# Kernel tuning notes

Hardware: AMD Instinct MI355X
Metric: run time of the kernel (lower is better)

The kernel has to match this reference:

```python
import jax, jax.numpy as jnp
import numpy as np

N = 10000
IN_DIM = 256
HID = 64


def gcn_norm(edge_index, num_nodes):
    # PyG gcn_norm with add_remaining_self_loops: drop existing self-loops
    # (weight 0), append one self-loop per node with weight 1, then
    # symmetric deg^-1/2 normalization.
    src, dst = edge_index[0], edge_index[1]
    w = jnp.where(src == dst, 0.0, 1.0).astype(jnp.float32)
    loops = jnp.arange(num_nodes, dtype=src.dtype)
    src_f = jnp.concatenate([src, loops])
    dst_f = jnp.concatenate([dst, loops])
    w_f = jnp.concatenate([w, jnp.ones((num_nodes,), jnp.float32)])
    deg = jax.ops.segment_sum(w_f, dst_f, num_segments=num_nodes)
    dinv = jnp.where(deg > 0, jax.lax.rsqrt(deg), 0.0)
    norm = dinv[src_f] * w_f * dinv[dst_f]
    return src_f, dst_f, norm


def gcn_conv(x, W, b, src, dst, norm, num_nodes):
    xw = x @ W                      # [N, out]
    msg = xw[src] * norm[:, None]   # gather + scale
    out = jax.ops.segment_sum(msg, dst, num_segments=num_nodes)
    return out + b


def setup_inputs() -> dict:
    key = jax.random.key(0)
    ks = jax.random.split(key, 16)
    x = jax.random.normal(ks[0], (N, IN_DIM), jnp.float32)
    edge_index = jax.random.randint(ks[1], (2, 320000), 0, N, dtype=jnp.int64)
    s = 0.1
    return {
        "x": x,
        "edge_index": edge_index,
        # shared_encoder: 2 layers, in->hid, hid->hid
        "enc_W1": jax.random.normal(ks[2], (IN_DIM, HID), jnp.float32) * s,
        "enc_b1": jnp.zeros((HID,), jnp.float32),
        "enc_W2": jax.random.normal(ks[3], (HID, HID), jnp.float32) * s,
        "enc_b2": jnp.zeros((HID,), jnp.float32),
        # attr_decoder: 2 layers, hid->hid, hid->in
        "attr_W1": jax.random.normal(ks[4], (HID, HID), jnp.float32) * s,
        "attr_b1": jnp.zeros((HID,), jnp.float32),
        "attr_W2": jax.random.normal(ks[5], (HID, IN_DIM), jnp.float32) * s,
        "attr_b2": jnp.zeros((IN_DIM,), jnp.float32),
        # struct_decoder: 1 layer, hid->in
        "struct_W": jax.random.normal(ks[6], (HID, IN_DIM), jnp.float32) * s,
        "struct_b": jnp.zeros((IN_DIM,), jnp.float32),
    }


def reference(x, edge_index, enc_W1, enc_b1, enc_W2, enc_b2,
              attr_W1, attr_b1, attr_W2, attr_b2, struct_W, struct_b):
    src, dst, norm = gcn_norm(edge_index, N)

    # shared encoder (relu between layers, none after last; dropout=0 eval)
    h = gcn_conv(x, enc_W1, enc_b1, src, dst, norm, N)
    h = jax.nn.relu(h)
    h = gcn_conv(h, enc_W2, enc_b2, src, dst, norm, N)

    # attribute decoder
    x_ = gcn_conv(h, attr_W1, attr_b1, src, dst, norm, N)
    x_ = jax.nn.relu(x_)
    x_ = gcn_conv(x_, attr_W2, attr_b2, src, dst, norm, N)

    # structure decoder + dense adjacency reconstruction
    h_ = gcn_conv(h, struct_W, struct_b, src, dst, norm, N)
    adj_ = h_ @ h_.T  # [N, N]
    return (x_, adj_)
```

## Files before the change

### kernel.cpp

```cpp
#include <hip/hip_runtime.h>
#include <hip/hip_bf16.h>

#define NN 10000
#define INDIM 256
#define HIDDIM 64

typedef __hip_bfloat16 bf16;
typedef unsigned short u16;
typedef __attribute__((ext_vector_type(8))) short bf16x8;
typedef __attribute__((ext_vector_type(4))) float f32x4;

__global__ void k_sniff(const unsigned* __restrict__ xw, const unsigned* __restrict__ ew,
                        int* __restrict__ flags) {
    if (threadIdx.x == 0 && blockIdx.x == 0) {
        int c = 0;
        for (int j = 0; j < 256; ++j) {
            unsigned e = (xw[j] >> 7) & 0xFF;
            c += (e >= 0x74 && e <= 0x85);
        }
        flags[0] = (c >= 128);
        int z = 0;
        for (int j = 0; j < 128; ++j) z += (ew[2 * j + 1] == 0u);
        flags[1] = (z >= 64);
    }
}

__global__ void k_cvt(const void* __restrict__ in, float* __restrict__ out, int n,
                      const int* __restrict__ flags) {
    int i = blockIdx.x * 256 + threadIdx.x;
    if (i >= n) return;
    if (flags[0]) out[i] = __bfloat162float(((const bf16*)in)[i]);
    else          out[i] = ((const float*)in)[i];
}

__global__ void k_cvt_idx(const void* __restrict__ ei, int* __restrict__ s32,
                          int* __restrict__ d32, int E, const int* __restrict__ flags) {
    int e = blockIdx.x * 256 + threadIdx.x;
    if (e >= E) return;
    if (flags[1]) {
        const long long* p = (const long long*)ei;
        s32[e] = (int)p[e]; d32[e] = (int)p[e + E];
    } else {
        const int* p = (const int*)ei;
        s32[e] = p[e]; d32[e] = p[e + E];
    }
}


__global__ void k_init_deg(float* deg) {
    int i = blockIdx.x * 256 + threadIdx.x;
    if (i < NN) deg[i] = 1.0f;
}

__global__ void k_edge_deg(const int* __restrict__ src, const int* __restrict__ dst,
                           float* __restrict__ deg, int E) {
    int e = blockIdx.x * 256 + threadIdx.x;
    if (e < E) {
        int s = src[e], d = dst[e];
        if (s != d) atomicAdd(&deg[d], 1.0f);
    }
}

__global__ void k_dinv(float* deg, float* selfn) {
    int i = blockIdx.x * 256 + threadIdx.x;
    if (i < NN) {
        float dv = 1.0f / sqrtf(deg[i]);
        deg[i] = dv;
        selfn[i] = dv * dv;
    }
}

__global__ void k_edge_norm(const int* __restrict__ src, const int* __restrict__ dst,
                            const float* __restrict__ dinv, float* __restrict__ nrm, int E) {
    int e = blockIdx.x * 256 + threadIdx.x;
    if (e < E) {
        int s = src[e], d = dst[e];
        nrm[e] = (s != d) ? dinv[s] * dinv[d] : 0.0f;
    }
}


template <int K, int NOUT>
__global__ void k_gemm(const float* __restrict__ A, const float* __restrict__ W,
                       float* __restrict__ out) {
    int j = blockIdx.x * 64 + threadIdx.x;
    int i = blockIdx.y * 4 + threadIdx.y;
    const float* arow = A + (size_t)i * K;
    float acc = 0.0f;
#pragma unroll 8
    for (int k = 0; k < K; ++k)
        acc = fmaf(arow[k], W[k * NOUT + j], acc);
    out[(size_t)i * NOUT + j] = acc;
}

template <int K, int NOUT, bool RELU>
__global__ void k_gemm_bias(const float* __restrict__ A, const float* __restrict__ W,
                            const float* __restrict__ b, float* __restrict__ out) {
    int j = blockIdx.x * 64 + threadIdx.x;
    int i = blockIdx.y * 4 + threadIdx.y;
    const float* arow = A + (size_t)i * K;
    float acc = b[j];
#pragma unroll 8
    for (int k = 0; k < K; ++k)
        acc = fmaf(arow[k], W[k * NOUT + j], acc);
    if (RELU) acc = fmaxf(acc, 0.0f);
    out[(size_t)i * NOUT + j] = acc;
}

__global__ void k_gemm_split(const float* __restrict__ A, const float* __restrict__ W,
                             const float* __restrict__ b,
                             u16* __restrict__ hi, u16* __restrict__ lo) {
    int j = blockIdx.x * 64 + threadIdx.x;
    int i = blockIdx.y * 4 + threadIdx.y;
    size_t o = (size_t)i * 256 + j;
    const float* arow = A + (size_t)i * 64;
    float acc = b[j];
#pragma unroll 8
    for (int k = 0; k < 64; ++k)
        acc = fmaf(arow[k], W[k * 256 + j], acc);
    bf16 h = __float2bfloat16(acc);
    float hf = __bfloat162float(h);
    bf16 l = __float2bfloat16(acc - hf);
    hi[o] = *(const u16*)&h;
    lo[o] = *(const u16*)&l;
}

__global__ void k_gemm_out(const float* __restrict__ A, const float* __restrict__ W,
                           const float* __restrict__ b, void* __restrict__ out,
                           const int* __restrict__ flags) {
    int j = blockIdx.x * 64 + threadIdx.x;
    int i = blockIdx.y * 4 + threadIdx.y;
    const float* arow = A + (size_t)i * 64;
    float acc = b[j];
#pragma unroll 8
    for (int k = 0; k < 64; ++k)
        acc = fmaf(arow[k], W[k * 256 + j], acc);
    size_t o = (size_t)i * 256 + j;
    if (flags[0]) ((bf16*)out)[o] = __float2bfloat16(acc);
    else          ((float*)out)[o] = acc;
}


template <int F>
__global__ void k_agg_init(const float* __restrict__ xw, const float* __restrict__ selfn,
                           float* __restrict__ agg) {
    int t = blockIdx.x * 256 + threadIdx.x;
    int i = t / F;
    agg[t] = selfn[i] * xw[t];
}

template <int F>
__global__ void k_scatter(const int* __restrict__ src, const int* __restrict__ dst,
                          const float* __restrict__ nrm, const float* __restrict__ xw,
                          float* __restrict__ agg, int E) {
    int e = blockIdx.x * 4 + (threadIdx.x >> 6);
    int lane = threadIdx.x & 63;
    if (e < E) {
        float w = nrm[e];
        if (w != 0.0f) {
            const float* xs = xw + (size_t)src[e] * F;
            float* ad = agg + (size_t)dst[e] * F;
#pragma unroll
            for (int r = 0; r < F / 64; ++r) {
                int f = r * 64 + lane;
                atomicAdd(ad + f, w * xs[f]);
            }
        }
    }
}

template <int F, bool RELU>
__global__ void k_finalize_f32(const float* __restrict__ agg, const float* __restrict__ b,
                               float* __restrict__ out) {
    int t = blockIdx.x * 256 + threadIdx.x;
    float v = agg[t] + b[t & (F - 1)];
    if (RELU) v = fmaxf(v, 0.0f);
    out[t] = v;
}


__global__ __launch_bounds__(256) void k_adj_mfma(const u16* __restrict__ hi,
                                                  const u16* __restrict__ lo,
                                                  void* __restrict__ d_out,
                                                  const int* __restrict__ flags) {
    int wid  = threadIdx.x >> 6;
    int lane = threadIdx.x & 63;
    int wr = wid >> 1, wc = wid & 1;
    int row0 = blockIdx.y * 128 + wr * 64;
    int col0 = blockIdx.x * 128 + wc * 64;
    int lr  = lane & 15;
    int klo = (lane >> 4) * 8;

    int aoff[4], boff[4];
#pragma unroll
    for (int u = 0; u < 4; ++u) {
        int r = row0 + u * 16 + lr; if (r > NN - 1) r = NN - 1;
        aoff[u] = r * 256 + klo;
        int c = col0 + u * 16 + lr; if (c > NN - 1) c = NN - 1;
        boff[u] = c * 256 + klo;
    }

    f32x4 acc[4][4] = {};
    for (int k0 = 0; k0 < 256; k0 += 32) {
        bf16x8 ah[4], al[4], bh[4], bl[4];
#pragma unroll
        for (int u = 0; u < 4; ++u) {
            ah[u] = *(const bf16x8*)(hi + aoff[u] + k0);
            al[u] = *(const bf16x8*)(lo + aoff[u] + k0);
            bh[u] = *(const bf16x8*)(hi + boff[u] + k0);
            bl[u] = *(const bf16x8*)(lo + boff[u] + k0);
        }
#pragma unroll
        for (int u = 0; u < 4; ++u)
#pragma unroll
            for (int v = 0; v < 4; ++v) {
                acc[u][v] = __builtin_amdgcn_mfma_f32_16x16x32_bf16(ah[u], bh[v], acc[u][v], 0, 0, 0);
                acc[u][v] = __builtin_amdgcn_mfma_f32_16x16x32_bf16(ah[u], bl[v], acc[u][v], 0, 0, 0);
                acc[u][v] = __builtin_amdgcn_mfma_f32_16x16x32_bf16(al[u], bh[v], acc[u][v], 0, 0, 0);
            }
    }

    int obf = flags[0];
    int cr = (lane >> 4) * 4;
    int cc = lane & 15;
    bf16*  ob = (bf16*)d_out + (size_t)NN * INDIM;
    float* of = (float*)d_out + (size_t)NN * INDIM;
#pragma unroll
    for (int u = 0; u < 4; ++u) {
#pragma unroll
        for (int r = 0; r < 4; ++r) {
            int i = row0 + u * 16 + cr + r;
            if (i >= NN) continue;
#pragma unroll
            for (int v = 0; v < 4; ++v) {
                int j = col0 + v * 16 + cc;
                if (j >= NN) continue;
                float val = acc[u][v][r];
                if (obf) ob[(size_t)i * NN + j] = __float2bfloat16(val);
                else     of[(size_t)i * NN + j] = val;
            }
        }
    }
}


extern "C" void kernel_launch(void* const* d_in, const int* in_sizes, int n_in,
                              void* d_out, int out_size, void* d_ws, size_t ws_size,
                              hipStream_t stream) {
    const void* x_raw  = d_in[0];
    const void* ei_raw = d_in[1];

    const int E = in_sizes[1] / 2;

    int*   flags = (int*)d_ws;
    float* wsf   = (float*)d_ws;
    float* deg   = wsf + 16;
    float* selfn = wsf + 10256;
    float* nrm   = wsf + 20496;
    int*   s32   = (int*)(wsf + 348176);
    int*   d32   = (int*)(wsf + 668176);
    float* w32   = wsf + 988176;
    u16*   hs_hi = (u16*)(wsf + 1046560);
    u16*   hs_lo = hs_hi + (size_t)NN * 256;

    float* encW1 = w32 + 0;
    float* encb1 = w32 + 16384;
    float* encW2 = w32 + 16448;
    float* encb2 = w32 + 20544;
    float* attW1 = w32 + 20608;
    float* attb1 = w32 + 24704;
    float* attW2 = w32 + 24768;
    float* attb2 = w32 + 41152;
    float* stW   = w32 + 41408;
    float* stb   = w32 + 57792;

    float* osc  = (float*)((char*)d_out + 16000000);
    float* x32  = osc;
    float* bufA = osc + 2560000;
    float* bufB = osc + 5120000;
    float* h1   = osc + 7680000;
    float* h2   = osc + 8320000;
    float* a1   = osc + 8960000;

    int eb  = (E + 255) / 256;
    int ewb = (E + 3) / 4;

    k_sniff<<<1, 64, 0, stream>>>((const unsigned*)x_raw, (const unsigned*)ei_raw, flags);

    k_cvt<<<10000, 256, 0, stream>>>(x_raw, x32, NN * INDIM, flags);
    k_cvt<<<64, 256, 0, stream>>>(d_in[2],  encW1, 16384, flags);
    k_cvt<<<1, 256, 0, stream>>>(d_in[3],   encb1, 64, flags);
    k_cvt<<<16, 256, 0, stream>>>(d_in[4],  encW2, 4096, flags);
    k_cvt<<<1, 256, 0, stream>>>(d_in[5],   encb2, 64, flags);
    k_cvt<<<16, 256, 0, stream>>>(d_in[6],  attW1, 4096, flags);
    k_cvt<<<1, 256, 0, stream>>>(d_in[7],   attb1, 64, flags);
    k_cvt<<<64, 256, 0, stream>>>(d_in[8],  attW2, 16384, flags);
    k_cvt<<<1, 256, 0, stream>>>(d_in[9],   attb2, 256, flags);
    k_cvt<<<64, 256, 0, stream>>>(d_in[10], stW, 16384, flags);
    k_cvt<<<1, 256, 0, stream>>>(d_in[11],  stb, 256, flags);
    k_cvt_idx<<<eb, 256, 0, stream>>>(ei_raw, s32, d32, E, flags);

    k_init_deg<<<40, 256, 0, stream>>>(deg);
    k_edge_deg<<<eb, 256, 0, stream>>>(s32, d32, deg, E);
    k_dinv<<<40, 256, 0, stream>>>(deg, selfn);
    k_edge_norm<<<eb, 256, 0, stream>>>(s32, d32, deg, nrm, E);

    k_gemm<256, 64><<<dim3(1, 2500), dim3(64, 4), 0, stream>>>(x32, encW1, bufA);
    k_agg_init<64><<<2500, 256, 0, stream>>>(bufA, selfn, bufB);
    k_scatter<64><<<ewb, 256, 0, stream>>>(s32, d32, nrm, bufA, bufB, E);
    k_finalize_f32<64, true><<<2500, 256, 0, stream>>>(bufB, encb1, h1);

    k_agg_init<64><<<2500, 256, 0, stream>>>(h1, selfn, bufB);
    k_scatter<64><<<ewb, 256, 0, stream>>>(s32, d32, nrm, h1, bufB, E);
    k_gemm_bias<64, 64, false><<<dim3(1, 2500), dim3(64, 4), 0, stream>>>(bufB, encW2, encb2, h2);

    k_agg_init<64><<<2500, 256, 0, stream>>>(h2, selfn, bufB);
    k_scatter<64><<<ewb, 256, 0, stream>>>(s32, d32, nrm, h2, bufB, E);
    k_gemm_bias<64, 64, true><<<dim3(1, 2500), dim3(64, 4), 0, stream>>>(bufB, attW1, attb1, a1);
    k_gemm_split<<<dim3(4, 2500), dim3(64, 4), 0, stream>>>(bufB, stW, stb, hs_hi, hs_lo);

    k_agg_init<64><<<2500, 256, 0, stream>>>(a1, selfn, bufB);
    k_scatter<64><<<ewb, 256, 0, stream>>>(s32, d32, nrm, a1, bufB, E);
    k_gemm_out<<<dim3(4, 2500), dim3(64, 4), 0, stream>>>(bufB, attW2, attb2, d_out, flags);

    k_adj_mfma<<<dim3(79, 79), 256, 0, stream>>>(hs_hi, hs_lo, d_out, flags);
}
```

Measured before the change: 1.322 ms.

## Replace atomic edge scatter with CSR gather and vectorize adjacency stores

```diff
diff --git a/kernel.cpp b/kernel.cpp
--- a/kernel.cpp
+++ b/kernel.cpp
@@ -9,6 +9,7 @@
 typedef unsigned short u16;
 typedef __attribute__((ext_vector_type(8))) short bf16x8;
 typedef __attribute__((ext_vector_type(4))) float f32x4;
+typedef __attribute__((ext_vector_type(4))) unsigned short u16x4;
 
 __global__ void k_sniff(const unsigned* __restrict__ xw, const unsigned* __restrict__ ew,
                         int* __restrict__ flags) {
@@ -33,49 +34,71 @@
     else          out[i] = ((const float*)in)[i];
 }
 
-__global__ void k_cvt_idx(const void* __restrict__ ei, int* __restrict__ s32,
-                          int* __restrict__ d32, int E, const int* __restrict__ flags) {
+__global__ void k_zero(int* __restrict__ p, int n) {
+    int i = blockIdx.x * 256 + threadIdx.x;
+    if (i < n) p[i] = 0;
+}
+
+__global__ void k_cvt_idx_count(const void* __restrict__ ei, int* __restrict__ s32,
+                                int* __restrict__ d32, int* __restrict__ cnt,
+                                int E, const int* __restrict__ flags) {
     int e = blockIdx.x * 256 + threadIdx.x;
     if (e >= E) return;
+    int s, d;
     if (flags[1]) {
         const long long* p = (const long long*)ei;
-        s32[e] = (int)p[e]; d32[e] = (int)p[e + E];
+        s = (int)p[e]; d = (int)p[e + E];
     } else {
         const int* p = (const int*)ei;
-        s32[e] = p[e]; d32[e] = p[e + E];
-    }
-}
-
-
-__global__ void k_init_deg(float* deg) {
-    int i = blockIdx.x * 256 + threadIdx.x;
-    if (i < NN) deg[i] = 1.0f;
-}
-
-__global__ void k_edge_deg(const int* __restrict__ src, const int* __restrict__ dst,
-                           float* __restrict__ deg, int E) {
+        s = p[e]; d = p[e + E];
+    }
+    s32[e] = s; d32[e] = d;
+    if (s != d) atomicAdd(&cnt[d], 1);
+}
+
+__global__ void k_scan(const int* __restrict__ cnt, int* __restrict__ off,
+                       int* __restrict__ cur, float* __restrict__ dinv,
+                       float* __restrict__ selfn) {
+    __shared__ int sums[256];
+    int t = threadIdx.x;
+    int base = t * 40;
+    int s = 0;
+    if (base < NN) {
+        int hi = base + 40; if (hi > NN) hi = NN;
+        for (int i = base; i < hi; ++i) s += cnt[i];
+    }
+    sums[t] = s;
+    __syncthreads();
+    for (int d = 1; d < 256; d <<= 1) {
+        int v = (t >= d) ? sums[t - d] : 0;
+        __syncthreads();
+        sums[t] += v;
+        __syncthreads();
+    }
+    int run = t ? sums[t - 1] : 0;
+    if (base < NN) {
+        int hi = base + 40; if (hi > NN) hi = NN;
+        for (int i = base; i < hi; ++i) {
+            off[i] = run; cur[i] = run;
+            int dg = cnt[i] + 1;
+            float dv = rsqrtf((float)dg);
+            dinv[i] = dv;
+            selfn[i] = 1.0f / (float)dg;
+            run += cnt[i];
+        }
+    }
+    if (t == 255) off[NN] = sums[255];
+}
+
+__global__ void k_fill(const int* __restrict__ s32, const int* __restrict__ d32,
+                       int* __restrict__ cur, int* __restrict__ csr, int E) {
     int e = blockIdx.x * 256 + threadIdx.x;
     if (e < E) {
-        int s = src[e], d = dst[e];
-        if (s != d) atomicAdd(&deg[d], 1.0f);
-    }
-}
-
-__global__ void k_dinv(float* deg, float* selfn) {
-    int i = blockIdx.x * 256 + threadIdx.x;
-    if (i < NN) {
-        float dv = 1.0f / sqrtf(deg[i]);
-        deg[i] = dv;
-        selfn[i] = dv * dv;
-    }
-}
-
-__global__ void k_edge_norm(const int* __restrict__ src, const int* __restrict__ dst,
-                            const float* __restrict__ dinv, float* __restrict__ nrm, int E) {
-    int e = blockIdx.x * 256 + threadIdx.x;
-    if (e < E) {
-        int s = src[e], d = dst[e];
-        nrm[e] = (s != d) ? dinv[s] * dinv[d] : 0.0f;
+        int s = s32[e], d = d32[e];
+        if (s != d) {
+            int p = atomicAdd(&cur[d], 1);
+            csr[p] = s;
+        }
     }
 }
 
@@ -141,41 +164,33 @@
 }
 
 
-template <int F>
-__global__ void k_agg_init(const float* __restrict__ xw, const float* __restrict__ selfn,
-                           float* __restrict__ agg) {
-    int t = blockIdx.x * 256 + threadIdx.x;
-    int i = t / F;
-    agg[t] = selfn[i] * xw[t];
-}
-
-template <int F>
-__global__ void k_scatter(const int* __restrict__ src, const int* __restrict__ dst,
-                          const float* __restrict__ nrm, const float* __restrict__ xw,
-                          float* __restrict__ agg, int E) {
-    int e = blockIdx.x * 4 + (threadIdx.x >> 6);
-    int lane = threadIdx.x & 63;
-    if (e < E) {
-        float w = nrm[e];
-        if (w != 0.0f) {
-            const float* xs = xw + (size_t)src[e] * F;
-            float* ad = agg + (size_t)dst[e] * F;
-#pragma unroll
-            for (int r = 0; r < F / 64; ++r) {
-                int f = r * 64 + lane;
-                atomicAdd(ad + f, w * xs[f]);
-            }
-        }
-    }
-}
-
-template <int F, bool RELU>
-__global__ void k_finalize_f32(const float* __restrict__ agg, const float* __restrict__ b,
-                               float* __restrict__ out) {
-    int t = blockIdx.x * 256 + threadIdx.x;
-    float v = agg[t] + b[t & (F - 1)];
-    if (RELU) v = fmaxf(v, 0.0f);
-    out[t] = v;
+template <bool BIASRELU>
+__global__ __launch_bounds__(256) void k_gather(const int* __restrict__ off,
+                                                const int* __restrict__ csr,
+                                                const float* __restrict__ dinv,
+                                                const float* __restrict__ selfn,
+                                                const float* __restrict__ xw,
+                                                const float* __restrict__ b,
+                                                float* __restrict__ out) {
+    int i = blockIdx.x * 4 + (threadIdx.x >> 6);
+    int f = threadIdx.x & 63;
+    float acc = selfn[i] * xw[(size_t)i * 64 + f];
+    int e = off[i], end = off[i + 1];
+    float di = dinv[i];
+    for (; e + 2 <= end; e += 2) {
+        int s0 = csr[e], s1 = csr[e + 1];
+        float w0 = di * dinv[s0], w1 = di * dinv[s1];
+        float v0 = xw[(size_t)s0 * 64 + f];
+        float v1 = xw[(size_t)s1 * 64 + f];
+        acc = fmaf(w0, v0, acc);
+        acc = fmaf(w1, v1, acc);
+    }
+    if (e < end) {
+        int s = csr[e];
+        acc = fmaf(di * dinv[s], xw[(size_t)s * 64 + f], acc);
+    }
+    if (BIASRELU) acc = fmaxf(acc + b[f], 0.0f);
+    out[(size_t)i * 64 + f] = acc;
 }
 
 
@@ -183,20 +198,26 @@
                                                   const u16* __restrict__ lo,
                                                   void* __restrict__ d_out,
                                                   const int* __restrict__ flags) {
+    const int NT = 79 * 79, q = NT / 8, r = NT % 8;
+    int orig = blockIdx.x;
+    int xcd = orig & 7, loc = orig >> 3;
+    int tile = (xcd < r ? xcd * (q + 1) : r * (q + 1) + (xcd - r) * q) + loc;
+    int by = tile / 79, bx = tile % 79;
+
     int wid  = threadIdx.x >> 6;
     int lane = threadIdx.x & 63;
     int wr = wid >> 1, wc = wid & 1;
-    int row0 = blockIdx.y * 128 + wr * 64;
-    int col0 = blockIdx.x * 128 + wc * 64;
+    int row0 = by * 128 + wr * 64;
+    int col0 = bx * 128 + wc * 64;
     int lr  = lane & 15;
     int klo = (lane >> 4) * 8;
 
     int aoff[4], boff[4];
 #pragma unroll
     for (int u = 0; u < 4; ++u) {
-        int r = row0 + u * 16 + lr; if (r > NN - 1) r = NN - 1;
-        aoff[u] = r * 256 + klo;
-        int c = col0 + u * 16 + lr; if (c > NN - 1) c = NN - 1;
+        int rr = row0 + u * 16 + lr; if (rr > NN - 1) rr = NN - 1;
+        aoff[u] = rr * 256 + klo;
+        int c = col0 + 4 * lr + u;   if (c > NN - 1) c = NN - 1;
         boff[u] = c * 256 + klo;
     }
 
@@ -223,21 +244,28 @@
     int obf = flags[0];
     int cr = (lane >> 4) * 4;
     int cc = lane & 15;
+    int j0 = col0 + 4 * cc;
     bf16*  ob = (bf16*)d_out + (size_t)NN * INDIM;
     float* of = (float*)d_out + (size_t)NN * INDIM;
-#pragma unroll
-    for (int u = 0; u < 4; ++u) {
-#pragma unroll
-        for (int r = 0; r < 4; ++r) {
-            int i = row0 + u * 16 + cr + r;
-            if (i >= NN) continue;
-#pragma unroll
-            for (int v = 0; v < 4; ++v) {
-                int j = col0 + v * 16 + cc;
-                if (j >= NN) continue;
-                float val = acc[u][v][r];
-                if (obf) ob[(size_t)i * NN + j] = __float2bfloat16(val);
-                else     of[(size_t)i * NN + j] = val;
+    if (j0 < NN) {
+#pragma unroll
+        for (int u = 0; u < 4; ++u) {
+#pragma unroll
+            for (int rr = 0; rr < 4; ++rr) {
+                int i = row0 + u * 16 + cr + rr;
+                if (i >= NN) continue;
+                if (obf) {
+                    u16x4 pv;
+#pragma unroll
+                    for (int v = 0; v < 4; ++v) {
+                        bf16 hb = __float2bfloat16(acc[u][v][rr]);
+                        pv[v] = *(const u16*)&hb;
+                    }
+                    __builtin_nontemporal_store(pv, (u16x4*)(ob + (size_t)i * NN + j0));
+                } else {
+                    f32x4 pv = { acc[u][0][rr], acc[u][1][rr], acc[u][2][rr], acc[u][3][rr] };
+                    __builtin_nontemporal_store(pv, (f32x4*)(of + (size_t)i * NN + j0));
+                }
             }
         }
     }
@@ -254,13 +282,12 @@
 
     int*   flags = (int*)d_ws;
     float* wsf   = (float*)d_ws;
-    float* deg   = wsf + 16;
+    float* dinv  = wsf + 16;
     float* selfn = wsf + 10256;
-    float* nrm   = wsf + 20496;
-    int*   s32   = (int*)(wsf + 348176);
-    int*   d32   = (int*)(wsf + 668176);
-    float* w32   = wsf + 988176;
-    u16*   hs_hi = (u16*)(wsf + 1046560);
+    int*   off   = (int*)(wsf + 20496);
+    int*   csr   = (int*)(wsf + 30752);
+    float* w32   = wsf + 358432;
+    u16*   hs_hi = (u16*)(wsf + 416480);
     u16*   hs_lo = hs_hi + (size_t)NN * 256;
 
     float* encW1 = w32 + 0;
@@ -277,13 +304,16 @@
     float* osc  = (float*)((char*)d_out + 16000000);
     float* x32  = osc;
     float* bufA = osc + 2560000;
-    float* bufB = osc + 5120000;
-    float* h1   = osc + 7680000;
-    float* h2   = osc + 8320000;
-    float* a1   = osc + 8960000;
-
-    int eb  = (E + 255) / 256;
-    int ewb = (E + 3) / 4;
+    float* bufB = osc + 3200000;
+    float* h1   = osc + 3840000;
+    float* h2   = osc + 4480000;
+    float* a1   = osc + 5120000;
+    int*   s32  = (int*)(osc + 5760000);
+    int*   d32  = (int*)(osc + 6087680);
+    int*   cnt  = (int*)(osc + 6415360);
+    int*   cur  = (int*)(osc + 6425600);
+
+    int eb = (E + 255) / 256;
 
     k_sniff<<<1, 64, 0, stream>>>((const unsigned*)x_raw, (const unsigned*)ei_raw, flags);
 
@@ -298,30 +328,24 @@
     k_cvt<<<1, 256, 0, stream>>>(d_in[9],   attb2, 256, flags);
     k_cvt<<<64, 256, 0, stream>>>(d_in[10], stW, 16384, flags);
     k_cvt<<<1, 256, 0, stream>>>(d_in[11],  stb, 256, flags);
-    k_cvt_idx<<<eb, 256, 0, stream>>>(ei_raw, s32, d32, E, flags);
-
-    k_init_deg<<<40, 256, 0, stream>>>(deg);
-    k_edge_deg<<<eb, 256, 0, stream>>>(s32, d32, deg, E);
-    k_dinv<<<40, 256, 0, stream>>>(deg, selfn);
-    k_edge_norm<<<eb, 256, 0, stream>>>(s32, d32, deg, nrm, E);
+
+    k_zero<<<40, 256, 0, stream>>>(cnt, 10240);
+    k_cvt_idx_count<<<eb, 256, 0, stream>>>(ei_raw, s32, d32, cnt, E, flags);
+    k_scan<<<1, 256, 0, stream>>>(cnt, off, cur, dinv, selfn);
+    k_fill<<<eb, 256, 0, stream>>>(s32, d32, cur, csr, E);
 
     k_gemm<256, 64><<<dim3(1, 2500), dim3(64, 4), 0, stream>>>(x32, encW1, bufA);
-    k_agg_init<64><<<2500, 256, 0, stream>>>(bufA, selfn, bufB);
-    k_scatter<64><<<ewb, 256, 0, stream>>>(s32, d32, nrm, bufA, bufB, E);
-    k_finalize_f32<64, true><<<2500, 256, 0, stream>>>(bufB, encb1, h1);
-
-    k_agg_init<64><<<2500, 256, 0, stream>>>(h1, selfn, bufB);
-    k_scatter<64><<<ewb, 256, 0, stream>>>(s32, d32, nrm, h1, bufB, E);
+    k_gather<true><<<2500, 256, 0, stream>>>(off, csr, dinv, selfn, bufA, encb1, h1);
+
+    k_gather<false><<<2500, 256, 0, stream>>>(off, csr, dinv, selfn, h1, encb1, bufB);
     k_gemm_bias<64, 64, false><<<dim3(1, 2500), dim3(64, 4), 0, stream>>>(bufB, encW2, encb2, h2);
 
-    k_agg_init<64><<<2500, 256, 0, stream>>>(h2, selfn, bufB);
-    k_scatter<64><<<ewb, 256, 0, stream>>>(s32, d32, nrm, h2, bufB, E);
+    k_gather<false><<<2500, 256, 0, stream>>>(off, csr, dinv, selfn, h2, encb1, bufB);
     k_gemm_bias<64, 64, true><<<dim3(1, 2500), dim3(64, 4), 0, stream>>>(bufB, attW1, attb1, a1);
     k_gemm_split<<<dim3(4, 2500), dim3(64, 4), 0, stream>>>(bufB, stW, stb, hs_hi, hs_lo);
 
-    k_agg_init<64><<<2500, 256, 0, stream>>>(a1, selfn, bufB);
-    k_scatter<64><<<ewb, 256, 0, stream>>>(s32, d32, nrm, a1, bufB, E);
+    k_gather<false><<<2500, 256, 0, stream>>>(off, csr, dinv, selfn, a1, encb1, bufB);
     k_gemm_out<<<dim3(4, 2500), dim3(64, 4), 0, stream>>>(bufB, attW2, attb2, d_out, flags);
 
-    k_adj_mfma<<<dim3(79, 79), 256, 0, stream>>>(hs_hi, hs_lo, d_out, flags);
-}
+    k_adj_mfma<<<6241, 256, 0, stream>>>(hs_hi, hs_lo, d_out, flags);
+}
```

Result: faster. 1.066 ms (-19.4%).
